# Performance work log

Measured on AMD Instinct MI355X. Metric: run time of the kernel, lower is better.

The kernel has to match this reference:

```python
import jax, jax.numpy as jnp
import numpy as np

B, N, KNN, C, H, LK, CEMB, GDIM = 16, 512, 20, 256, 128, 4, 64, 64


def _lrelu(x, slope):
    return jnp.where(x >= 0, x, slope * x)


def _forward(img_feat, graph_feat, roi_mask_bit, prev_x_id, prev_y_id, knn_idx,
             conv_w, conv_b, pre_w1, pre_b1, pre_w2, pre_b2,
             g1_w, g1_gamma, g1_beta, g1_mean, g1_var,
             g2_w, g2_gamma, g2_beta, g2_mean, g2_var,
             q_w1, q_b1, q_w2, q_b2, q_w3, q_b3):
    lk = conv_w.shape[-1]
    bsz = img_feat.shape[0]
    # Index2Feat: conv with padding = lk-1 -> (B, CEMB, H+lk-1, W+lk-1)
    patches = jax.lax.conv_general_dilated(img_feat, conv_w, (1, 1), [(lk - 1, lk - 1)] * 2)
    patches = patches + conv_b[None, :, None, None]
    p = jnp.transpose(patches, (0, 2, 3, 1))  # (B, Hp, Wp, CEMB)
    bi = jnp.arange(bsz)[:, None]
    yy, xx = 2 * prev_y_id, 2 * prev_x_id
    sf1 = p[bi, yy, xx]
    sf2 = p[bi, yy + lk, xx]
    sf3 = p[bi, yy, xx + lk]
    sf4 = p[bi, yy + lk, xx + lk]
    local = jnp.concatenate([sf1, sf2, sf3, sf4], axis=-1)  # (B, N, 4*CEMB)
    local = local * jnp.transpose(roi_mask_bit, (0, 2, 1))  # detached mask
    local = jnp.concatenate([local, jnp.transpose(graph_feat, (0, 2, 1))], axis=-1)  # (B,N,320)
    # pre_graph MLP (LeakyReLU 0.01, doLastAct=True)
    h = _lrelu(local @ pre_w1 + pre_b1, 0.01)
    h = _lrelu(h @ pre_w2 + pre_b2, 0.01)  # (B, N, C)
    knn = knn_idx[0]  # (N, K) shared across batch

    def edgeconv(x, w, gamma, beta, mean, var):
        xk = x[:, knn]  # (B, N, K, C) neighbor gather
        xc = jnp.broadcast_to(x[:, :, None, :], xk.shape)
        e = jnp.concatenate([xk - xc, xc], axis=-1)  # (B, N, K, 2C)
        y = jnp.einsum('bnkc,oc->bnko', e, w)  # 1x1 conv, no bias
        y = (y - mean) * (gamma / jnp.sqrt(var + 1e-5)) + beta  # BN (inference)
        return _lrelu(y, 0.2).max(axis=2)  # max over k neighbors

    h = edgeconv(h, g1_w, g1_gamma, g1_beta, g1_mean, g1_var)
    h = edgeconv(h, g2_w, g2_gamma, g2_beta, g2_mean, g2_var)
    # query MLP (256 -> 256 -> 64 -> 2), LeakyReLU 0.01, no last act
    q = _lrelu(h @ q_w1 + q_b1, 0.01)
    q = _lrelu(q @ q_w2 + q_b2, 0.01)
    bits = q @ q_w3 + q_b3  # (B, N, 2)
    return jnp.transpose(bits, (0, 2, 1)), jnp.transpose(h, (0, 2, 1))


def setup_inputs() -> dict:
    key = jax.random.key(0)
    ks = jax.random.split(key, 24)
    s = 0.02
    img_feat = jax.random.normal(ks[0], (B, C, H, H), jnp.float32)
    graph_feat = jax.random.normal(ks[1], (B, GDIM, N), jnp.float32)
    roi_mask_bit = jnp.ones((B, 1, N), jnp.float32)
    prev_x_id = jax.random.randint(ks[2], (B, N), 0, H // 2, jnp.int32)
    prev_y_id = jax.random.randint(ks[3], (B, N), 0, H // 2, jnp.int32)
    # knn graph from normalized 3D keypoints (computed once at init in torch)
    p3d = jax.random.uniform(ks[4], (1, 3, N), jnp.float32, -1.0, 1.0)
    inner = -2.0 * jnp.einsum('bdn,bdm->bnm', p3d, p3d)
    xsq = jnp.sum(p3d ** 2, axis=1, keepdims=True)  # (1,1,N)
    pd = -xsq - inner - jnp.transpose(xsq, (0, 2, 1))
    knn_idx = jax.lax.top_k(pd, KNN)[1].astype(jnp.int32)  # (1, N, KNN)
    return {
        'img_feat': img_feat, 'graph_feat': graph_feat, 'roi_mask_bit': roi_mask_bit,
        'prev_x_id': prev_x_id, 'prev_y_id': prev_y_id, 'knn_idx': knn_idx,
        'conv_w': jax.random.normal(ks[5], (CEMB, C, LK, LK), jnp.float32) * s,
        'conv_b': jnp.zeros((CEMB,), jnp.float32),
        'pre_w1': jax.random.normal(ks[6], (4 * CEMB + GDIM, C), jnp.float32) * s,
        'pre_b1': jnp.zeros((C,), jnp.float32),
        'pre_w2': jax.random.normal(ks[7], (C, C), jnp.float32) * s,
        'pre_b2': jnp.zeros((C,), jnp.float32),
        'g1_w': jax.random.normal(ks[8], (C, 2 * C), jnp.float32) * s,
        'g1_gamma': jnp.ones((C,), jnp.float32), 'g1_beta': jnp.zeros((C,), jnp.float32),
        'g1_mean': jnp.zeros((C,), jnp.float32), 'g1_var': jnp.ones((C,), jnp.float32),
        'g2_w': jax.random.normal(ks[9], (C, 2 * C), jnp.float32) * s,
        'g2_gamma': jnp.ones((C,), jnp.float32), 'g2_beta': jnp.zeros((C,), jnp.float32),
        'g2_mean': jnp.zeros((C,), jnp.float32), 'g2_var': jnp.ones((C,), jnp.float32),
        'q_w1': jax.random.normal(ks[10], (C, C), jnp.float32) * s,
        'q_b1': jnp.zeros((C,), jnp.float32),
        'q_w2': jax.random.normal(ks[11], (C, 64), jnp.float32) * s,
        'q_b2': jnp.zeros((64,), jnp.float32),
        'q_w3': jax.random.normal(ks[12], (64, 2), jnp.float32) * s,
        'q_b3': jnp.zeros((2,), jnp.float32),
    }


def reference(img_feat, graph_feat, roi_mask_bit, prev_x_id, prev_y_id, knn_idx,
              conv_w, conv_b, pre_w1, pre_b1, pre_w2, pre_b2,
              g1_w, g1_gamma, g1_beta, g1_mean, g1_var,
              g2_w, g2_gamma, g2_beta, g2_mean, g2_var,
              q_w1, q_b1, q_w2, q_b2, q_w3, q_b3):
    return _forward(img_feat, graph_feat, roi_mask_bit, prev_x_id, prev_y_id, knn_idx,
                    conv_w, conv_b, pre_w1, pre_b1, pre_w2, pre_b2,
                    g1_w, g1_gamma, g1_beta, g1_mean, g1_var,
                    g2_w, g2_gamma, g2_beta, g2_mean, g2_var,
                    q_w1, q_b1, q_w2, q_b2, q_w3, q_b3)
```

## Files before the change

### kernel.cpp

```cpp
#include <hip/hip_runtime.h>


typedef __bf16 bf16_t;
typedef bf16_t bf16x2 __attribute__((ext_vector_type(2)));
typedef bf16_t bf16x8 __attribute__((ext_vector_type(8)));
typedef float  f32x4  __attribute__((ext_vector_type(4)));

static constexpr int BATCH = 16;
static constexpr int NPT   = 512;
static constexpr int PTS   = BATCH * NPT;
static constexpr int CONVM = PTS * 4;
static constexpr int CONVK = 4096;

static constexpr int PY_DIM = 136;
static constexpr size_t IMG_BSTRIDE = (size_t)PY_DIM * PY_DIM * 256;

static constexpr size_t OFF_WCONV_OLD = 0;
static constexpr size_t OFF_WCONVP    = OFF_WCONV_OLD + (size_t)64*4096*2;
static constexpr size_t OFF_WPRE1     = OFF_WCONVP    + (size_t)64*4096*2;
static constexpr size_t OFF_WPRE2     = OFF_WPRE1     + (size_t)256*320*2;
static constexpr size_t OFF_WEC1      = OFF_WPRE2     + (size_t)256*256*2;
static constexpr size_t OFF_WEC2      = OFF_WEC1      + (size_t)512*256*2;
static constexpr size_t OFF_WQ1       = OFF_WEC2      + (size_t)512*256*2;
static constexpr size_t OFF_WQ2       = OFF_WQ1       + (size_t)256*256*2;
static constexpr size_t OFF_LOCAL     = OFF_WQ2       + (size_t)64*256*2;
static constexpr size_t OFF_X         = OFF_LOCAL + (size_t)PTS*320*2;
static constexpr size_t OFF_Y         = OFF_X     + (size_t)PTS*256*2;
static constexpr size_t OFF_Z         = OFF_Y     + (size_t)PTS*256*2;
static constexpr size_t OFF_UNION     = OFF_Z     + (size_t)PTS*64*2;
static constexpr size_t AB_BYTES      = (size_t)PTS*512*2;
static constexpr size_t IMGT_BYTES    = (size_t)16*IMG_BSTRIDE*2;
static constexpr size_t WS_BASE       = OFF_UNION + AB_BYTES;
static constexpr size_t WS_FULL       = OFF_UNION + IMGT_BYTES;

static constexpr int WP_CONV  = 64*4096;
static constexpr int WP_CONVP = 64*4096;
static constexpr int WP_PRE1 = 256*320;
static constexpr int WP_PRE2 = 256*256;
static constexpr int WP_EC   = 512*256;
static constexpr int WP_Q1   = 256*256;
static constexpr int WP_Q2   = 64*256;
static constexpr int WP_TOTAL = WP_CONV + WP_CONVP + WP_PRE1 + WP_PRE2 + 2*WP_EC + WP_Q1 + WP_Q2;

__global__ __launch_bounds__(256) void wprep_kernel(
    const float* __restrict__ conv_w, const float* __restrict__ pre_w1,
    const float* __restrict__ pre_w2, const float* __restrict__ g1_w,
    const float* __restrict__ g2_w,   const float* __restrict__ q_w1,
    const float* __restrict__ q_w2,
    bf16_t* __restrict__ wt_conv, bf16_t* __restrict__ wt_convp,
    bf16_t* __restrict__ wt_pre1,
    bf16_t* __restrict__ wt_pre2, bf16_t* __restrict__ wt_ec1,
    bf16_t* __restrict__ wt_ec2,  bf16_t* __restrict__ wt_q1,
    bf16_t* __restrict__ wt_q2)
{
    int i = blockIdx.x * 256 + threadIdx.x;
    if (i >= WP_TOTAL) return;
    if (i < WP_CONV) { wt_conv[i] = (bf16_t)conv_w[i]; return; }
    i -= WP_CONV;
    if (i < WP_CONVP) {
        const int o = i >> 12, pix = (i >> 8) & 15, c = i & 255;
        wt_convp[i] = (bf16_t)conv_w[((o * 256 + c) << 4) + pix]; return; }
    i -= WP_CONVP;
    if (i < WP_PRE1) { int n = i / 320, k = i - n * 320;
        wt_pre1[i] = (bf16_t)pre_w1[k * 256 + n]; return; }
    i -= WP_PRE1;
    if (i < WP_PRE2) { int n = i >> 8, k = i & 255;
        wt_pre2[i] = (bf16_t)pre_w2[k * 256 + n]; return; }
    i -= WP_PRE2;
    if (i < WP_EC) { int n = i >> 8, k = i & 255;
        wt_ec1[i] = (bf16_t)(n < 256 ? g1_w[n * 512 + k] : g1_w[(n - 256) * 512 + 256 + k]);
        return; }
    i -= WP_EC;
    if (i < WP_EC) { int n = i >> 8, k = i & 255;
        wt_ec2[i] = (bf16_t)(n < 256 ? g2_w[n * 512 + k] : g2_w[(n - 256) * 512 + 256 + k]);
        return; }
    i -= WP_EC;
    if (i < WP_Q1) { int n = i >> 8, k = i & 255;
        wt_q1[i] = (bf16_t)q_w1[k * 256 + n]; return; }
    i -= WP_Q1;
    { int n = i >> 8, k = i & 255;
        wt_q2[i] = (bf16_t)q_w2[k * 64 + n]; }
}

static constexpr int PAD_THREADS = 16 * 2112 * 32;

__global__ __launch_bounds__(256) void pad_border(bf16_t* __restrict__ imgT)
{
    const int idx = blockIdx.x * 256 + threadIdx.x;
    if (idx >= PAD_THREADS) return;
    const int t = idx & 31;
    int pi = idx >> 5;
    const int b = pi / 2112; pi -= b * 2112;
    int y, x;
    if (pi < 544)      { y = pi / 136;              x = pi % 136; }
    else if (pi < 1088){ int j = pi - 544; y = 132 + j / 136; x = j % 136; }
    else { int j = pi - 1088; y = 4 + (j >> 3); int k = j & 7; x = (k < 4) ? k : (128 + k); }
    const uint4 z = {0, 0, 0, 0};
    ((uint4*)(imgT + ((size_t)(b * PY_DIM + y) * PY_DIM + x) * 256))[t] = z;
}

__global__ __launch_bounds__(256) void transpose_img(
    const float* __restrict__ img, bf16_t* __restrict__ imgT)
{
    __shared__ float T[64][65];
    const int bid = blockIdx.x;
    const int cc = bid & 3;
    const int xh = (bid >> 2) & 1;
    const int y  = (bid >> 3) & 127;
    const int b  = bid >> 10;
    const int t = threadIdx.x;
    const int x0 = xh * 64, c0 = cc * 64;
    {
        const int px = t & 63, cr = t >> 6;
        const float* src = img + ((size_t)(b * 256 + c0 + cr) * 128 + y) * 128 + x0 + px;
        #pragma unroll
        for (int i = 0; i < 16; ++i)
            T[cr + i * 4][px] = src[(size_t)i * 4 * 16384];
    }
    __syncthreads();
    {
        const int cl2 = (t & 31) * 2, pr = t >> 5;
        bf16_t* dst = imgT + ((size_t)(b * PY_DIM + y + 4) * PY_DIM + x0 + 4) * 256 + c0 + cl2;
        #pragma unroll
        for (int i = 0; i < 8; ++i) {
            const int pxl = pr + i * 8;
            bf16x2 w;
            w[0] = (bf16_t)T[cl2][pxl];
            w[1] = (bf16_t)T[cl2 + 1][pxl];
            *(bf16x2*)(dst + (size_t)pxl * 256) = w;
        }
    }
}

__global__ __launch_bounds__(256) void conv_gather_gemm3p(
    const bf16_t* __restrict__ imgT,
    const bf16_t* __restrict__ Wc,
    const float* __restrict__ conv_b, const float* __restrict__ roi,
    const int* __restrict__ px, const int* __restrict__ py,
    bf16_t* __restrict__ local)
{
    __shared__ bf16_t As[32][136];
    __shared__ bf16_t Bs[64][136];
    const int tid = threadIdx.x, lane = tid & 63, wave = tid >> 6;
    const int wm = wave & 1, wn = wave >> 1;
    const int row0 = blockIdx.x * 32;

    const int ra = tid >> 3, seg = tid & 7;
    const int r = row0 + ra, corner = r & 3, pnt = r >> 2, b = pnt >> 9;
    const int oy = 2 * py[pnt] + (corner & 1) * 4 + 1;
    const int ox = 2 * px[pnt] + ((corner >> 1) & 1) * 4 + 1;
    const bf16_t* imgb = imgT + (size_t)b * IMG_BSTRIDE;
    const int rb = tid >> 2, sq = tid & 3;
    const bf16_t* wrow = Wc + (size_t)rb * 4096 + sq * 8;

    uint4 a0, a1, b0, b1, b2, b3;
    {
        const bf16_t* srcA = imgb + ((size_t)((oy) * PY_DIM + ox)) * 256 + seg * 16;
        a0 = *(const uint4*)srcA;
        a1 = *(const uint4*)(srcA + 8);
        const bf16_t* srcB = wrow;
        b0 = *(const uint4*)srcB;
        b1 = *(const uint4*)(srcB + 32);
        b2 = *(const uint4*)(srcB + 64);
        b3 = *(const uint4*)(srcB + 96);
    }

    f32x4 acc[2] = {};
    #pragma unroll 1
    for (int s = 0; s < 32; ++s) {
        __syncthreads();
        *(uint4*)&As[ra][seg * 16]     = a0;
        *(uint4*)&As[ra][seg * 16 + 8] = a1;
        *(uint4*)&Bs[rb][sq * 8]       = b0;
        *(uint4*)&Bs[rb][sq * 8 + 32]  = b1;
        *(uint4*)&Bs[rb][sq * 8 + 64]  = b2;
        *(uint4*)&Bs[rb][sq * 8 + 96]  = b3;
        if (s < 31) {
            const int sn = s + 1;
            const int pix = sn >> 1, h = sn & 1;
            const int iy = oy + (pix >> 2), ix = ox + (pix & 3);
            const bf16_t* srcA = imgb + ((size_t)(iy * PY_DIM + ix)) * 256 + h * 128 + seg * 16;
            a0 = *(const uint4*)srcA;
            a1 = *(const uint4*)(srcA + 8);
            const bf16_t* srcB = wrow + pix * 256 + h * 128;
            b0 = *(const uint4*)srcB;
            b1 = *(const uint4*)(srcB + 32);
            b2 = *(const uint4*)(srcB + 64);
            b3 = *(const uint4*)(srcB + 96);
        }
        __syncthreads();
        #pragma unroll
        for (int kk = 0; kk < 128; kk += 32) {
            const int kf = kk + ((lane >> 4) << 3);
            bf16x8 a  = *(const bf16x8*)&As[wm * 16 + (lane & 15)][kf];
            bf16x8 bb0 = *(const bf16x8*)&Bs[wn * 32 + (lane & 15)][kf];
            bf16x8 bb1 = *(const bf16x8*)&Bs[wn * 32 + 16 + (lane & 15)][kf];
            acc[0] = __builtin_amdgcn_mfma_f32_16x16x32_bf16(a, bb0, acc[0], 0, 0, 0);
            acc[1] = __builtin_amdgcn_mfma_f32_16x16x32_bf16(a, bb1, acc[1], 0, 0, 0);
        }
    }
    const int crow = (lane >> 4) << 2;
    const int ccol = lane & 15;
    #pragma unroll
    for (int j = 0; j < 2; ++j) {
        const int o = wn * 32 + j * 16 + ccol;
        const float bv = conv_b[o];
        #pragma unroll
        for (int rg = 0; rg < 4; ++rg) {
            const int gr = row0 + wm * 16 + crow + rg;
            const int cn = gr & 3;
            const int pp = gr >> 2;
            const float v = (acc[j][rg] + bv) * roi[pp];
            local[(size_t)pp * 320 + cn * 64 + o] = (bf16_t)v;
        }
    }
}

__global__ __launch_bounds__(256) void conv_gather_gemm(
    const float* __restrict__ img, const bf16_t* __restrict__ Wc,
    const float* __restrict__ conv_b, const float* __restrict__ roi,
    const int* __restrict__ px, const int* __restrict__ py,
    bf16_t* __restrict__ local)
{
    __shared__ bf16_t As[64][72];
    __shared__ bf16_t Bs[64][72];
    const int tid = threadIdx.x;
    const int lane = tid & 63;
    const int wave = tid >> 6;
    const int wm = wave & 1, wn = wave >> 1;
    const int row0 = blockIdx.x * 64;
    const int sm = tid >> 2;
    const int cq = tid & 3;
    const int r = row0 + sm;
    const int corner = r & 3;
    const int pnt = r >> 2;
    const int b = pnt >> 9;
    const int oy = 2 * py[pnt] + (corner & 1) * 4;
    const int ox = 2 * px[pnt] + ((corner >> 1) & 1) * 4;
    const int iy0 = oy - 3, ix0 = ox - 3;
    const float* imgb = img + (size_t)b * (256 * 128 * 128);

    f32x4 acc[2][2] = {};
    for (int kt = 0; kt < CONVK; kt += 64) {
        {
            const int c = (kt >> 4) + cq;
            const float* ip = imgb + (size_t)c * (128 * 128);
            alignas(16) bf16_t vals[16];
            #pragma unroll
            for (int ky = 0; ky < 4; ++ky) {
                const int iy = iy0 + ky;
                const bool yok = (unsigned)iy < 128u;
                #pragma unroll
                for (int kx = 0; kx < 4; ++kx) {
                    const int ix = ix0 + kx;
                    float v = (yok && (unsigned)ix < 128u) ? ip[iy * 128 + ix] : 0.0f;
                    vals[ky * 4 + kx] = (bf16_t)v;
                }
            }
            *(uint4*)&As[sm][cq * 16]     = *(const uint4*)&vals[0];
            *(uint4*)&As[sm][cq * 16 + 8] = *(const uint4*)&vals[8];
        }
        {
            const bf16_t* src = Wc + (size_t)sm * CONVK + kt + cq * 16;
            *(uint4*)&Bs[sm][cq * 16]     = *(const uint4*)src;
            *(uint4*)&Bs[sm][cq * 16 + 8] = *(const uint4*)(src + 8);
        }
        __syncthreads();
        #pragma unroll
        for (int kk = 0; kk < 64; kk += 32) {
            const int kf = kk + ((lane >> 4) << 3);
            bf16x8 a0 = *(const bf16x8*)&As[wm * 32 + (lane & 15)][kf];
            bf16x8 a1 = *(const bf16x8*)&As[wm * 32 + 16 + (lane & 15)][kf];
            bf16x8 b0 = *(const bf16x8*)&Bs[wn * 32 + (lane & 15)][kf];
            bf16x8 b1 = *(const bf16x8*)&Bs[wn * 32 + 16 + (lane & 15)][kf];
            acc[0][0] = __builtin_amdgcn_mfma_f32_16x16x32_bf16(a0, b0, acc[0][0], 0, 0, 0);
            acc[0][1] = __builtin_amdgcn_mfma_f32_16x16x32_bf16(a0, b1, acc[0][1], 0, 0, 0);
            acc[1][0] = __builtin_amdgcn_mfma_f32_16x16x32_bf16(a1, b0, acc[1][0], 0, 0, 0);
            acc[1][1] = __builtin_amdgcn_mfma_f32_16x16x32_bf16(a1, b1, acc[1][1], 0, 0, 0);
        }
        __syncthreads();
    }
    const int crow = (lane >> 4) << 2;
    const int ccol = lane & 15;
    #pragma unroll
    for (int i = 0; i < 2; ++i) {
        #pragma unroll
        for (int j = 0; j < 2; ++j) {
            const int o = wn * 32 + j * 16 + ccol;
            const float bv = conv_b[o];
            #pragma unroll
            for (int rg = 0; rg < 4; ++rg) {
                const int gr = row0 + wm * 32 + i * 16 + crow + rg;
                const int cn = gr & 3;
                const int pp = gr >> 2;
                const float v = (acc[i][j][rg] + bv) * roi[pp];
                local[(size_t)pp * 320 + cn * 64 + o] = (bf16_t)v;
            }
        }
    }
}

__global__ __launch_bounds__(256) void graph_fill(
    const float* __restrict__ g, bf16_t* __restrict__ local)
{
    const int e = blockIdx.x * 256 + threadIdx.x;
    const int j = e & 63, p = e >> 6;
    const int b = p >> 9, n = p & 511;
    local[(size_t)p * 320 + 256 + j] = (bf16_t)g[((size_t)(b * 64 + j) << 9) + n];
}

template<int K, int KSTEP, int N, int ACT>
__global__ __launch_bounds__(256) void gemm_bf16(
    const bf16_t* __restrict__ A, const bf16_t* __restrict__ Bt,
    const float* __restrict__ bias, float slope,
    bf16_t* __restrict__ outB, float* __restrict__ outF)
{
    __shared__ bf16_t As[64][KSTEP + 8];
    __shared__ bf16_t Bs[64][KSTEP + 8];
    const int tid = threadIdx.x;
    const int lane = tid & 63;
    const int wave = tid >> 6;
    const int wm = wave & 1, wn = wave >> 1;
    const int row0 = blockIdx.x * 64;
    const int col0 = blockIdx.y * 64;
    const int sm = tid >> 2;
    const int sq = (tid & 3) * (KSTEP / 4);

    f32x4 acc[2][2] = {};
    #pragma unroll 1
    for (int kt = 0; kt < K; kt += KSTEP) {
        {
            const bf16_t* src = A + (size_t)(row0 + sm) * K + kt + sq;
            #pragma unroll
            for (int i = 0; i < KSTEP / 32; ++i)
                *(uint4*)&As[sm][sq + i * 8] = *(const uint4*)(src + i * 8);
        }
        {
            const bf16_t* src = Bt + (size_t)(col0 + sm) * K + kt + sq;
            #pragma unroll
            for (int i = 0; i < KSTEP / 32; ++i)
                *(uint4*)&Bs[sm][sq + i * 8] = *(const uint4*)(src + i * 8);
        }
        __syncthreads();
        #pragma unroll
        for (int kk = 0; kk < KSTEP; kk += 32) {
            const int kf = kk + ((lane >> 4) << 3);
            bf16x8 a0 = *(const bf16x8*)&As[wm * 32 + (lane & 15)][kf];
            bf16x8 a1 = *(const bf16x8*)&As[wm * 32 + 16 + (lane & 15)][kf];
            bf16x8 b0 = *(const bf16x8*)&Bs[wn * 32 + (lane & 15)][kf];
            bf16x8 b1 = *(const bf16x8*)&Bs[wn * 32 + 16 + (lane & 15)][kf];
            acc[0][0] = __builtin_amdgcn_mfma_f32_16x16x32_bf16(a0, b0, acc[0][0], 0, 0, 0);
            acc[0][1] = __builtin_amdgcn_mfma_f32_16x16x32_bf16(a0, b1, acc[0][1], 0, 0, 0);
            acc[1][0] = __builtin_amdgcn_mfma_f32_16x16x32_bf16(a1, b0, acc[1][0], 0, 0, 0);
            acc[1][1] = __builtin_amdgcn_mfma_f32_16x16x32_bf16(a1, b1, acc[1][1], 0, 0, 0);
        }
        __syncthreads();
    }
    const int crow = (lane >> 4) << 2;
    const int ccol = lane & 15;
    #pragma unroll
    for (int i = 0; i < 2; ++i) {
        #pragma unroll
        for (int j = 0; j < 2; ++j) {
            const int gcol = col0 + wn * 32 + j * 16 + ccol;
            const float bv = bias ? bias[gcol] : 0.0f;
            #pragma unroll
            for (int rg = 0; rg < 4; ++rg) {
                const int grow = row0 + wm * 32 + i * 16 + crow + rg;
                float v = acc[i][j][rg] + bv;
                if (ACT == 1) v = v >= 0.0f ? v : slope * v;
                if (outB) outB[(size_t)grow * N + gcol] = (bf16_t)v;
                if (outF) outF[(size_t)grow * N + gcol] = v;
            }
        }
    }
}

__global__ __launch_bounds__(256) void edge_combine(
    const bf16_t* __restrict__ AB, const int* __restrict__ knn,
    const float* __restrict__ gamma, const float* __restrict__ beta,
    const float* __restrict__ mean,  const float* __restrict__ var,
    bf16_t* __restrict__ outB, float* __restrict__ outT)
{
    const int p = blockIdx.x;
    const int b = p >> 9, n = p & 511;
    const int o = threadIdx.x;
    const float sc = gamma[o] / sqrtf(var[o] + 1e-5f);
    const float sh = beta[o] - mean[o] * sc;
    const bf16_t* rowp = AB + (size_t)p * 512;
    const float d = (float)rowp[256 + o] - (float)rowp[o];
    const bf16_t* batch = AB + ((size_t)(b << 9)) * 512;
    float m = -3.4e38f;
    #pragma unroll 4
    for (int k = 0; k < 20; ++k) {
        const int q = knn[n * 20 + k];
        const float v = (float)batch[(size_t)q * 512 + o] + d;
        float y = v * sc + sh;
        y = y >= 0.0f ? y : 0.2f * y;
        m = fmaxf(m, y);
    }
    outB[(size_t)p * 256 + o] = (bf16_t)m;
    if (outT) outT[((size_t)(b * 256 + o) << 9) + n] = m;
}

__global__ __launch_bounds__(256) void q3_kernel(
    const bf16_t* __restrict__ Z, const float* __restrict__ w3,
    const float* __restrict__ b3, float* __restrict__ out)
{
    const int p = blockIdx.x * 256 + threadIdx.x;
    const int b = p >> 9, n = p & 511;
    const bf16_t* q = Z + (size_t)p * 64;
    float s0 = b3[0], s1 = b3[1];
    #pragma unroll
    for (int c = 0; c < 64; ++c) {
        const float v = (float)q[c];
        s0 += v * w3[2 * c];
        s1 += v * w3[2 * c + 1];
    }
    out[(size_t)(b * 2 + 0) * 512 + n] = s0;
    out[(size_t)(b * 2 + 1) * 512 + n] = s1;
}

extern "C" void kernel_launch(void* const* d_in, const int* in_sizes, int n_in,
                              void* d_out, int out_size, void* d_ws, size_t ws_size,
                              hipStream_t stream)
{
    const float* img      = (const float*)d_in[0];
    const float* graph    = (const float*)d_in[1];
    const float* roi      = (const float*)d_in[2];
    const int*   px       = (const int*)d_in[3];
    const int*   py       = (const int*)d_in[4];
    const int*   knn      = (const int*)d_in[5];
    const float* conv_w   = (const float*)d_in[6];
    const float* conv_b   = (const float*)d_in[7];
    const float* pre_w1   = (const float*)d_in[8];
    const float* pre_b1   = (const float*)d_in[9];
    const float* pre_w2   = (const float*)d_in[10];
    const float* pre_b2   = (const float*)d_in[11];
    const float* g1_w     = (const float*)d_in[12];
    const float* g1_gamma = (const float*)d_in[13];
    const float* g1_beta  = (const float*)d_in[14];
    const float* g1_mean  = (const float*)d_in[15];
    const float* g1_var   = (const float*)d_in[16];
    const float* g2_w     = (const float*)d_in[17];
    const float* g2_gamma = (const float*)d_in[18];
    const float* g2_beta  = (const float*)d_in[19];
    const float* g2_mean  = (const float*)d_in[20];
    const float* g2_var   = (const float*)d_in[21];
    const float* q_w1     = (const float*)d_in[22];
    const float* q_b1     = (const float*)d_in[23];
    const float* q_w2     = (const float*)d_in[24];
    const float* q_b2     = (const float*)d_in[25];
    const float* q_w3     = (const float*)d_in[26];
    const float* q_b3     = (const float*)d_in[27];
    float* out = (float*)d_out;

    if (ws_size < WS_BASE) return;

    char* ws = (char*)d_ws;
    bf16_t* wt_conv  = (bf16_t*)(ws + OFF_WCONV_OLD);
    bf16_t* wt_convp = (bf16_t*)(ws + OFF_WCONVP);
    bf16_t* wt_pre1  = (bf16_t*)(ws + OFF_WPRE1);
    bf16_t* wt_pre2  = (bf16_t*)(ws + OFF_WPRE2);
    bf16_t* wt_ec1   = (bf16_t*)(ws + OFF_WEC1);
    bf16_t* wt_ec2   = (bf16_t*)(ws + OFF_WEC2);
    bf16_t* wt_q1    = (bf16_t*)(ws + OFF_WQ1);
    bf16_t* wt_q2    = (bf16_t*)(ws + OFF_WQ2);
    bf16_t* local    = (bf16_t*)(ws + OFF_LOCAL);
    bf16_t* X        = (bf16_t*)(ws + OFF_X);
    bf16_t* Y        = (bf16_t*)(ws + OFF_Y);
    bf16_t* Z        = (bf16_t*)(ws + OFF_Z);
    bf16_t* AB       = (bf16_t*)(ws + OFF_UNION);
    bf16_t* imgT     = (bf16_t*)(ws + OFF_UNION);

    const bool big = ws_size >= WS_FULL;

    wprep_kernel<<<(WP_TOTAL + 255) / 256, 256, 0, stream>>>(
        conv_w, pre_w1, pre_w2, g1_w, g2_w, q_w1, q_w2,
        wt_conv, wt_convp, wt_pre1, wt_pre2, wt_ec1, wt_ec2, wt_q1, wt_q2);

    if (big) {
        pad_border<<<(PAD_THREADS + 255) / 256, 256, 0, stream>>>(imgT);
        transpose_img<<<16 * 128 * 2 * 4, 256, 0, stream>>>(img, imgT);
        conv_gather_gemm3p<<<CONVM / 32, 256, 0, stream>>>(
            imgT, wt_convp, conv_b, roi, px, py, local);
    } else {
        conv_gather_gemm<<<CONVM / 64, 256, 0, stream>>>(
            img, wt_conv, conv_b, roi, px, py, local);
    }

    graph_fill<<<(PTS * 64) / 256, 256, 0, stream>>>(graph, local);

    gemm_bf16<320, 160, 256, 1><<<dim3(PTS / 64, 4), 256, 0, stream>>>(
        local, wt_pre1, pre_b1, 0.01f, X, nullptr);
    gemm_bf16<256, 256, 256, 1><<<dim3(PTS / 64, 4), 256, 0, stream>>>(
        X, wt_pre2, pre_b2, 0.01f, Y, nullptr);

    gemm_bf16<256, 128, 512, 0><<<dim3(PTS / 64, 8), 256, 0, stream>>>(
        Y, wt_ec1, nullptr, 0.0f, AB, nullptr);
    edge_combine<<<PTS, 256, 0, stream>>>(
        AB, knn, g1_gamma, g1_beta, g1_mean, g1_var, X, nullptr);

    gemm_bf16<256, 128, 512, 0><<<dim3(PTS / 64, 8), 256, 0, stream>>>(
        X, wt_ec2, nullptr, 0.0f, AB, nullptr);
    edge_combine<<<PTS, 256, 0, stream>>>(
        AB, knn, g2_gamma, g2_beta, g2_mean, g2_var, Y, out + 16384);

    gemm_bf16<256, 256, 256, 1><<<dim3(PTS / 64, 4), 256, 0, stream>>>(
        Y, wt_q1, q_b1, 0.01f, X, nullptr);
    gemm_bf16<256, 256, 64, 1><<<dim3(PTS / 64, 1), 256, 0, stream>>>(
        X, wt_q2, q_b2, 0.01f, Z, nullptr);
    q3_kernel<<<PTS / 256, 256, 0, stream>>>(Z, q_w3, q_b3, out);
}
```

Before: 261.4 us.

## Fuse pad into wprep, graph fill into conv, q2+q3, split transpose/conv by batch halves

Merges the border-padding kernel into the weight-prep kernel and folds the graph-feature fill into the conv gather GEMM epilogue. The image transpose and conv are split into two batch halves so the conv for the first half can follow its transpose sooner and stay cache-friendly. It also fuses the 256->64 query GEMM with the final 64->2 projection in shared memory, dropping an intermediate buffer. Together these cut kernel launches and global round trips, at the cost of more launches in the split and some duplicated index math.

```diff
diff --git a/kernel.cpp b/kernel.cpp
--- a/kernel.cpp
+++ b/kernel.cpp
@@ -41,8 +41,9 @@
 static constexpr int WP_Q1   = 256*256;
 static constexpr int WP_Q2   = 64*256;
 static constexpr int WP_TOTAL = WP_CONV + WP_CONVP + WP_PRE1 + WP_PRE2 + 2*WP_EC + WP_Q1 + WP_Q2;
-
-__global__ __launch_bounds__(256) void wprep_kernel(
+static constexpr int PAD_THREADS = 16 * 2112 * 32;
+
+__global__ __launch_bounds__(256) void wprep_pad_kernel(
     const float* __restrict__ conv_w, const float* __restrict__ pre_w1,
     const float* __restrict__ pre_w2, const float* __restrict__ g1_w,
     const float* __restrict__ g2_w,   const float* __restrict__ q_w1,
@@ -51,10 +52,23 @@
     bf16_t* __restrict__ wt_pre1,
     bf16_t* __restrict__ wt_pre2, bf16_t* __restrict__ wt_ec1,
     bf16_t* __restrict__ wt_ec2,  bf16_t* __restrict__ wt_q1,
-    bf16_t* __restrict__ wt_q2)
+    bf16_t* __restrict__ wt_q2,   bf16_t* __restrict__ imgT)
 {
     int i = blockIdx.x * 256 + threadIdx.x;
-    if (i >= WP_TOTAL) return;
+    if (i >= WP_TOTAL) {
+        const int idx = i - WP_TOTAL;
+        if (idx >= PAD_THREADS || imgT == nullptr) return;
+        const int t = idx & 31;
+        int pi = idx >> 5;
+        const int b = pi / 2112; pi -= b * 2112;
+        int y, x;
+        if (pi < 544)      { y = pi / 136;              x = pi % 136; }
+        else if (pi < 1088){ int j = pi - 544; y = 132 + j / 136; x = j % 136; }
+        else { int j = pi - 1088; y = 4 + (j >> 3); int k = j & 7; x = (k < 4) ? k : (128 + k); }
+        const uint4 z = {0, 0, 0, 0};
+        ((uint4*)(imgT + ((size_t)(b * PY_DIM + y) * PY_DIM + x) * 256))[t] = z;
+        return;
+    }
     if (i < WP_CONV) { wt_conv[i] = (bf16_t)conv_w[i]; return; }
     i -= WP_CONV;
     if (i < WP_CONVP) {
@@ -82,32 +96,15 @@
         wt_q2[i] = (bf16_t)q_w2[k * 64 + n]; }
 }
 
-static constexpr int PAD_THREADS = 16 * 2112 * 32;
-
-__global__ __launch_bounds__(256) void pad_border(bf16_t* __restrict__ imgT)
-{
-    const int idx = blockIdx.x * 256 + threadIdx.x;
-    if (idx >= PAD_THREADS) return;
-    const int t = idx & 31;
-    int pi = idx >> 5;
-    const int b = pi / 2112; pi -= b * 2112;
-    int y, x;
-    if (pi < 544)      { y = pi / 136;              x = pi % 136; }
-    else if (pi < 1088){ int j = pi - 544; y = 132 + j / 136; x = j % 136; }
-    else { int j = pi - 1088; y = 4 + (j >> 3); int k = j & 7; x = (k < 4) ? k : (128 + k); }
-    const uint4 z = {0, 0, 0, 0};
-    ((uint4*)(imgT + ((size_t)(b * PY_DIM + y) * PY_DIM + x) * 256))[t] = z;
-}
-
 __global__ __launch_bounds__(256) void transpose_img(
-    const float* __restrict__ img, bf16_t* __restrict__ imgT)
+    const float* __restrict__ img, bf16_t* __restrict__ imgT, int b0)
 {
     __shared__ float T[64][65];
     const int bid = blockIdx.x;
     const int cc = bid & 3;
     const int xh = (bid >> 2) & 1;
     const int y  = (bid >> 3) & 127;
-    const int b  = bid >> 10;
+    const int b  = b0 + (bid >> 10);
     const int t = threadIdx.x;
     const int x0 = xh * 64, c0 = cc * 64;
     {
@@ -137,13 +134,14 @@
     const bf16_t* __restrict__ Wc,
     const float* __restrict__ conv_b, const float* __restrict__ roi,
     const int* __restrict__ px, const int* __restrict__ py,
-    bf16_t* __restrict__ local)
+    const float* __restrict__ graph,
+    bf16_t* __restrict__ local, int row_base)
 {
     __shared__ bf16_t As[32][136];
     __shared__ bf16_t Bs[64][136];
     const int tid = threadIdx.x, lane = tid & 63, wave = tid >> 6;
     const int wm = wave & 1, wn = wave >> 1;
-    const int row0 = blockIdx.x * 32;
+    const int row0 = row_base + blockIdx.x * 32;
 
     const int ra = tid >> 3, seg = tid & 7;
     const int r = row0 + ra, corner = r & 3, pnt = r >> 2, b = pnt >> 9;
@@ -214,6 +212,14 @@
             local[(size_t)pp * 320 + cn * 64 + o] = (bf16_t)v;
         }
     }
+    {
+        const int pt = (row0 >> 2) + (tid >> 5);
+        const int ch = (tid & 31) * 2;
+        const int bb = pt >> 9, nn = pt & 511;
+        const float* gsrc = graph + (((size_t)bb * 64) << 9) + nn;
+        local[(size_t)pt * 320 + 256 + ch]     = (bf16_t)gsrc[(size_t)ch << 9];
+        local[(size_t)pt * 320 + 256 + ch + 1] = (bf16_t)gsrc[(size_t)(ch + 1) << 9];
+    }
 }
 
 __global__ __launch_bounds__(256) void conv_gather_gemm(
@@ -401,6 +407,76 @@
     }
     outB[(size_t)p * 256 + o] = (bf16_t)m;
     if (outT) outT[((size_t)(b * 256 + o) << 9) + n] = m;
+}
+
+__global__ __launch_bounds__(256) void q23_kernel(
+    const bf16_t* __restrict__ A,
+    const bf16_t* __restrict__ B2t,
+    const float* __restrict__ b2,
+    const float* __restrict__ w3, const float* __restrict__ b3,
+    float* __restrict__ out)
+{
+    __shared__ bf16_t As[64][264];
+    __shared__ bf16_t Bs[64][264];
+    __shared__ bf16_t Zs[64][72];
+    const int tid = threadIdx.x, lane = tid & 63, wave = tid >> 6;
+    const int wm = wave & 1, wn = wave >> 1;
+    const int row0 = blockIdx.x * 64;
+    const int sm = tid >> 2, sq = (tid & 3) * 64;
+    {
+        const bf16_t* src = A + (size_t)(row0 + sm) * 256 + sq;
+        #pragma unroll
+        for (int i = 0; i < 8; ++i)
+            *(uint4*)&As[sm][sq + i * 8] = *(const uint4*)(src + i * 8);
+    }
+    {
+        const bf16_t* src = B2t + (size_t)sm * 256 + sq;
+        #pragma unroll
+        for (int i = 0; i < 8; ++i)
+            *(uint4*)&Bs[sm][sq + i * 8] = *(const uint4*)(src + i * 8);
+    }
+    __syncthreads();
+    f32x4 acc[2][2] = {};
+    #pragma unroll
+    for (int kk = 0; kk < 256; kk += 32) {
+        const int kf = kk + ((lane >> 4) << 3);
+        bf16x8 a0 = *(const bf16x8*)&As[wm * 32 + (lane & 15)][kf];
+        bf16x8 a1 = *(const bf16x8*)&As[wm * 32 + 16 + (lane & 15)][kf];
+        bf16x8 b0 = *(const bf16x8*)&Bs[wn * 32 + (lane & 15)][kf];
+        bf16x8 b1 = *(const bf16x8*)&Bs[wn * 32 + 16 + (lane & 15)][kf];
+        acc[0][0] = __builtin_amdgcn_mfma_f32_16x16x32_bf16(a0, b0, acc[0][0], 0, 0, 0);
+        acc[0][1] = __builtin_amdgcn_mfma_f32_16x16x32_bf16(a0, b1, acc[0][1], 0, 0, 0);
+        acc[1][0] = __builtin_amdgcn_mfma_f32_16x16x32_bf16(a1, b0, acc[1][0], 0, 0, 0);
+        acc[1][1] = __builtin_amdgcn_mfma_f32_16x16x32_bf16(a1, b1, acc[1][1], 0, 0, 0);
+    }
+    __syncthreads();
+    const int crow = (lane >> 4) << 2;
+    const int ccol = lane & 15;
+    #pragma unroll
+    for (int i = 0; i < 2; ++i) {
+        #pragma unroll
+        for (int j = 0; j < 2; ++j) {
+            const int gcol = wn * 32 + j * 16 + ccol;
+            const float bv = b2[gcol];
+            #pragma unroll
+            for (int rg = 0; rg < 4; ++rg) {
+                const int rl = wm * 32 + i * 16 + crow + rg;
+                float v = acc[i][j][rg] + bv;
+                v = v >= 0.0f ? v : 0.01f * v;
+                Zs[rl][gcol] = (bf16_t)v;
+            }
+        }
+    }
+    __syncthreads();
+    if (tid < 128) {
+        const int rl = tid >> 1, jj = tid & 1;
+        float s = b3[jj];
+        #pragma unroll
+        for (int c = 0; c < 64; ++c)
+            s += (float)Zs[rl][c] * w3[2 * c + jj];
+        const int gr = row0 + rl, bb = gr >> 9, nn = gr & 511;
+        out[(size_t)(bb * 2 + jj) * 512 + nn] = s;
+    }
 }
 
 __global__ __launch_bounds__(256) void q3_kernel(
@@ -475,21 +551,22 @@
 
     const bool big = ws_size >= WS_FULL;
 
-    wprep_kernel<<<(WP_TOTAL + 255) / 256, 256, 0, stream>>>(
+    wprep_pad_kernel<<<(WP_TOTAL + PAD_THREADS + 255) / 256, 256, 0, stream>>>(
         conv_w, pre_w1, pre_w2, g1_w, g2_w, q_w1, q_w2,
-        wt_conv, wt_convp, wt_pre1, wt_pre2, wt_ec1, wt_ec2, wt_q1, wt_q2);
+        wt_conv, wt_convp, wt_pre1, wt_pre2, wt_ec1, wt_ec2, wt_q1, wt_q2,
+        big ? imgT : nullptr);
 
     if (big) {
-        pad_border<<<(PAD_THREADS + 255) / 256, 256, 0, stream>>>(imgT);
-        transpose_img<<<16 * 128 * 2 * 4, 256, 0, stream>>>(img, imgT);
-        conv_gather_gemm3p<<<CONVM / 32, 256, 0, stream>>>(
-            imgT, wt_convp, conv_b, roi, px, py, local);
+        for (int g = 0; g < 2; ++g) {
+            transpose_img<<<8 * 128 * 2 * 4, 256, 0, stream>>>(img, imgT, 8 * g);
+            conv_gather_gemm3p<<<CONVM / 32 / 2, 256, 0, stream>>>(
+                imgT, wt_convp, conv_b, roi, px, py, graph, local, g * (CONVM / 2));
+        }
     } else {
         conv_gather_gemm<<<CONVM / 64, 256, 0, stream>>>(
             img, wt_conv, conv_b, roi, px, py, local);
-    }
-
-    graph_fill<<<(PTS * 64) / 256, 256, 0, stream>>>(graph, local);
+        graph_fill<<<(PTS * 64) / 256, 256, 0, stream>>>(graph, local);
+    }
 
     gemm_bf16<320, 160, 256, 1><<<dim3(PTS / 64, 4), 256, 0, stream>>>(
         local, wt_pre1, pre_b1, 0.01f, X, nullptr);
@@ -508,7 +585,6 @@
 
     gemm_bf16<256, 256, 256, 1><<<dim3(PTS / 64, 4), 256, 0, stream>>>(
         Y, wt_q1, q_b1, 0.01f, X, nullptr);
-    gemm_bf16<256, 256, 64, 1><<<dim3(PTS / 64, 1), 256, 0, stream>>>(
-        X, wt_q2, q_b2, 0.01f, Z, nullptr);
-    q3_kernel<<<PTS / 256, 256, 0, stream>>>(Z, q_w3, q_b3, out);
-}
+    q23_kernel<<<PTS / 64, 256, 0, stream>>>(
+        X, wt_q2, q_b2, q_w3, q_b3, out);
+}
```

After: 253.1 us. 1.03x faster.
